# Optimization experiments

Measured on AMD Instinct MI355X. Metric: run time of the kernel, lower is better.

## Reference

```python
import jax, jax.numpy as jnp
import numpy as np
import math

D_MODEL = 128      # embedding_dim
D_STATE = 64
D_CONV = 4
NHEADS = 4         # d_inner / headdim (Mamba2 default headdim=64)
HEADDIM = 64
D_INNER = 256      # expand * d_model
CONV_DIM = 384     # d_inner + 2*ngroups*d_state (ngroups=1)
D_IN_PROJ = 644    # 2*d_inner + 2*ngroups*d_state + nheads
NLAYERS = 2
INPUT_DIM = 768
EPS = 1e-5


def setup_inputs() -> dict:
    key = jax.random.key(0)
    ks = jax.random.split(key, 20)
    rn = lambda k, s, sd=0.02: jax.random.normal(k, s, jnp.float32) * sd
    return {
        "x": jax.random.normal(ks[0], (16, 1024, INPUT_DIM), jnp.float32),
        "fc1_W": rn(ks[1], (INPUT_DIM, D_MODEL)),
        "fc1_b": jnp.zeros((D_MODEL,), jnp.float32),
        "ln_w": jnp.ones((NLAYERS, D_MODEL), jnp.float32),
        "ln_b": jnp.zeros((NLAYERS, D_MODEL), jnp.float32),
        "in_W": rn(ks[2], (NLAYERS, D_MODEL, D_IN_PROJ)),
        "conv_w": rn(ks[3], (NLAYERS, D_CONV, CONV_DIM), 0.1),
        "conv_b": jnp.zeros((NLAYERS, CONV_DIM), jnp.float32),
        "dt_bias": rn(ks[4], (NLAYERS, NHEADS), 0.5),
        "A_log": jnp.log(jax.random.uniform(ks[5], (NLAYERS, NHEADS), jnp.float32, 1.0, 16.0)),
        "Dp": jnp.ones((NLAYERS, NHEADS), jnp.float32),
        "rms_w": jnp.ones((NLAYERS, D_INNER), jnp.float32),
        "out_W": rn(ks[6], (NLAYERS, D_INNER, D_MODEL)),
        "fc2_W1": rn(ks[7], (D_MODEL, D_MODEL)),
        "fc2_b1": jnp.zeros((D_MODEL,), jnp.float32),
        "fc2_W2": rn(ks[8], (D_MODEL, 6)),
        "fc2_b2": jnp.zeros((6,), jnp.float32),
    }


def _pos_embedding(L):
    pos = jnp.arange(L, dtype=jnp.float32)[:, None]                       # (L,1)
    div = jnp.exp(jnp.arange(0, D_MODEL, 2, dtype=jnp.float32) * (-math.log(10000.0) / D_MODEL))
    pe = jnp.zeros((L, D_MODEL), jnp.float32)
    pe = pe.at[:, 0::2].set(jnp.sin(pos * div))
    pe = pe.at[:, 1::2].set(jnp.cos(pos * div))
    return pe[None]                                                        # (1,L,D)


def _layernorm(x, w, b):
    mu = jnp.mean(x, -1, keepdims=True)
    var = jnp.mean(jnp.square(x - mu), -1, keepdims=True)
    return (x - mu) * jax.lax.rsqrt(var + EPS) * w + b


def _mamba2(u, in_W, conv_w, conv_b, dt_bias, A_log, Dp, rms_w, out_W):
    b, l, _ = u.shape
    zxbcdt = u @ in_W                                                      # (b,l,644)
    z = zxbcdt[..., :D_INNER]
    xBC = zxbcdt[..., D_INNER:D_INNER + CONV_DIM]
    dt = jax.nn.softplus(zxbcdt[..., D_INNER + CONV_DIM:] + dt_bias)       # (b,l,h)
    # causal depthwise conv1d (width 4) + SiLU
    xp = jnp.pad(xBC, ((0, 0), (D_CONV - 1, 0), (0, 0)))
    xc = conv_b
    for k in range(D_CONV):
        xc = xc + conv_w[k] * xp[:, k:k + l, :]
    xc = jax.nn.silu(xc)                                                   # (b,l,384)
    xh = xc[..., :D_INNER].reshape(b, l, NHEADS, HEADDIM)                  # (b,l,h,p)
    B = xc[..., D_INNER:D_INNER + D_STATE]                                 # (b,l,n)
    C = xc[..., D_INNER + D_STATE:]                                        # (b,l,n)
    A = -jnp.exp(A_log)                                                    # (h,)
    dA = jnp.exp(dt * A)                                                   # (b,l,h)
    dtx = dt[..., None] * xh                                               # (b,l,h,p)

    def step(h, inp):
        dA_t, dtx_t, B_t, C_t = inp                                        # (b,h),(b,h,p),(b,n),(b,n)
        h = dA_t[..., None, None] * h + dtx_t[..., None] * B_t[:, None, None, :]
        y = jnp.einsum('bhpn,bn->bhp', h, C_t)
        return h, y

    h0 = jnp.zeros((b, NHEADS, HEADDIM, D_STATE), u.dtype)
    _, ys = jax.lax.scan(step, h0, (dA.transpose(1, 0, 2), dtx.transpose(1, 0, 2, 3),
                                    B.transpose(1, 0, 2), C.transpose(1, 0, 2)))
    y = ys.transpose(1, 0, 2, 3) + Dp[None, None, :, None] * xh            # (b,l,h,p)
    y = y.reshape(b, l, D_INNER)
    # gated RMSNorm: rmsnorm(y * silu(z)) * weight
    y = y * jax.nn.silu(z)
    y = y * jax.lax.rsqrt(jnp.mean(jnp.square(y), -1, keepdims=True) + EPS) * rms_w
    return y @ out_W


def reference(x, fc1_W, fc1_b, ln_w, ln_b, in_W, conv_w, conv_b, dt_bias,
              A_log, Dp, rms_w, out_W, fc2_W1, fc2_b1, fc2_W2, fc2_b2):
    h = x @ fc1_W + fc1_b                                                  # (b,l,128)
    h = h + _pos_embedding(h.shape[1])
    for i in range(NLAYERS):
        res = h
        hn = _layernorm(h, ln_w[i], ln_b[i])
        h = _mamba2(hn, in_W[i], conv_w[i], conv_b[i], dt_bias[i],
                    A_log[i], Dp[i], rms_w[i], out_W[i]) + res
        # dropout: identity in eval mode
    h = jax.nn.leaky_relu(h @ fc2_W1 + fc2_b1, negative_slope=0.1)
    return h @ fc2_W2 + fc2_b2                                             # (b,l,6)
```

## Files before the change

### kernel.cpp

```cpp
#include <hip/hip_runtime.h>
#include <hip/hip_bf16.h>

#define BATCH 16
#define SEQ 1024
#define NROWS (BATCH*SEQ)
#define IN_DIM 768
#define DM 128
#define DIP 644
#define DI 256
#define CDIM 384
#define DST 64
#define NH 4
#define HD 64
#define CHUNK 64
#define NCHUNK (SEQ/CHUNK)

#define WB_FC1   0
#define WB_IN    98304
#define WB_OUT   263168
#define WB_FC2   328704
#define WB_TOTAL 345088

typedef __attribute__((ext_vector_type(8))) short short8;
typedef __attribute__((ext_vector_type(4))) float float4v;

__device__ __forceinline__ short f2b(float f) {
    unsigned u = __builtin_bit_cast(unsigned, f);
    u += 0x7fffu + ((u >> 16) & 1u);
    return (short)(u >> 16);
}
__device__ __forceinline__ float s2f(short s) {
    unsigned u = ((unsigned)(unsigned short)s) << 16;
    return __builtin_bit_cast(float, u);
}
__device__ __forceinline__ float silu(float a) { return a / (1.f + expf(-a)); }

__global__ void prep_weights(const float* __restrict__ fc1_W, const float* __restrict__ in_W,
                             const float* __restrict__ out_W, const float* __restrict__ fc2_W1,
                             short* __restrict__ wb) {
    int idx = blockIdx.x * 256 + threadIdx.x;
    if (idx < 98304) {
        int n = idx / 768, k = idx % 768;
        wb[WB_FC1 + idx] = f2b(fc1_W[k * 128 + n]);
        return;
    }
    idx -= 98304;
    if (idx < 2 * 82432) {
        int l = idx / 82432, r = idx % 82432;
        int n = r / 128, k = r % 128;
        wb[WB_IN + idx] = f2b(in_W[(size_t)l * 82432 + k * 644 + n]);
        return;
    }
    idx -= 164864;
    if (idx < 2 * 32768) {
        int l = idx / 32768, r = idx % 32768;
        int n = r / 256, k = r % 256;
        wb[WB_OUT + idx] = f2b(out_W[(size_t)l * 32768 + k * 128 + n]);
        return;
    }
    idx -= 65536;
    if (idx < 16384) {
        int n = idx / 128, k = idx % 128;
        wb[WB_FC2 + idx] = f2b(fc2_W1[k * 128 + n]);
    }
}

#define GEMM_PROLOGUE() \
    int tid = threadIdx.x; \
    int lane = tid & 63; \
    int m = lane & 15; \
    int kq = (lane >> 4) * 8; \
    int w = tid >> 6; \
    int mrow = (w & 3) * 16; \
    int ngrp = w >> 2; \
    int a_off = (mrow + m) * 72 + kq; \
    int b_off = (ngrp * 64 + m) * 72 + kq; \
    int ar = tid >> 3; \
    int ak = (tid & 7) * 8; \
    (void)ar; (void)ak; \
    float4v acc[4]; \
    acc[0] = (float4v)0.f; acc[1] = (float4v)0.f; acc[2] = (float4v)0.f; acc[3] = (float4v)0.f;

#define GEMM_COMPUTE_TILE() \
    { \
        short8 a0 = *reinterpret_cast<const short8*>(&As[a_off]); \
        short8 a1 = *reinterpret_cast<const short8*>(&As[a_off + 32]); \
        _Pragma("unroll") \
        for (int nt = 0; nt < 4; nt++) { \
            short8 b0 = *reinterpret_cast<const short8*>(&Bt[b_off + nt * 16 * 72]); \
            short8 b1 = *reinterpret_cast<const short8*>(&Bt[b_off + nt * 16 * 72 + 32]); \
            acc[nt] = __builtin_amdgcn_mfma_f32_16x16x32_bf16(a0, b0, acc[nt], 0, 0, 0); \
            acc[nt] = __builtin_amdgcn_mfma_f32_16x16x32_bf16(a1, b1, acc[nt], 0, 0, 0); \
        } \
    }

__global__ __launch_bounds__(512) void fc1_mfma(const float* __restrict__ x,
                                                const short* __restrict__ wt,
                                                const float* __restrict__ bias,
                                                const float* __restrict__ lnw0,
                                                const float* __restrict__ lnb0,
                                                float* __restrict__ h,
                                                short* __restrict__ hnb) {
    __shared__ short As[2][32 * 72];
    __shared__ short Bt[2][128 * 72];
    __shared__ float ps1[32][4], ps2[32][4];
    int tid = threadIdx.x;
    int lane = tid & 63;
    int m = lane & 15;
    int quad = lane >> 4;
    int kq = quad * 8;
    int w = tid >> 6;
    int mrow = (w & 1) * 16;
    int ngrp = w >> 1;
    int ar = tid >> 4;
    int ac = (tid & 15) * 4;
    int row0 = blockIdx.x * 32;
    float4v acc[2];
    acc[0] = (float4v)0.f; acc[1] = (float4v)0.f;

#define FC1_STAGE(BI, KT) { \
        const float* src = x + (size_t)(row0 + ar) * IN_DIM + (KT) * 64 + ac; \
        float4 v = *(const float4*)src; \
        short4 pv; pv.x = f2b(v.x); pv.y = f2b(v.y); pv.z = f2b(v.z); pv.w = f2b(v.w); \
        *reinterpret_cast<short4*>(&As[BI][ar * 72 + ac]) = pv; \
        _Pragma("unroll") \
        for (int i = 0; i < 2; i++) { \
            int idx = tid + i * 512; \
            int n = idx >> 3, kk = (idx & 7) * 8; \
            *reinterpret_cast<short8*>(&Bt[BI][n * 72 + kk]) = \
                *reinterpret_cast<const short8*>(&wt[n * 768 + (KT) * 64 + kk]); \
        } }

    FC1_STAGE(0, 0)
    __syncthreads();
    int buf = 0;
    for (int kt = 0; kt < 12; kt++) {
        int nb = buf ^ 1;
        if (kt < 11) FC1_STAGE(nb, kt + 1)
        short8 a0 = *reinterpret_cast<const short8*>(&As[buf][(mrow + m) * 72 + kq]);
        short8 a1 = *reinterpret_cast<const short8*>(&As[buf][(mrow + m) * 72 + kq + 32]);
        #pragma unroll
        for (int nt = 0; nt < 2; nt++) {
            int bo = (ngrp * 32 + nt * 16 + m) * 72 + kq;
            short8 b0 = *reinterpret_cast<const short8*>(&Bt[buf][bo]);
            short8 b1 = *reinterpret_cast<const short8*>(&Bt[buf][bo + 32]);
            acc[nt] = __builtin_amdgcn_mfma_f32_16x16x32_bf16(a0, b0, acc[nt], 0, 0, 0);
            acc[nt] = __builtin_amdgcn_mfma_f32_16x16x32_bf16(a1, b1, acc[nt], 0, 0, 0);
        }
        __syncthreads();
        buf = nb;
    }
    float val[2][4];
    float s1r[4] = {0.f,0.f,0.f,0.f}, s2r[4] = {0.f,0.f,0.f,0.f};
    #pragma unroll
    for (int nt = 0; nt < 2; nt++) {
        int col = ngrp * 32 + nt * 16 + m;
        float bv = bias[col];
        float div = expf(-(float)(col & ~1) * 0.071955784f);
        #pragma unroll
        for (int r = 0; r < 4; r++) {
            int row = row0 + mrow + quad * 4 + r;
            int t = row & (SEQ - 1);
            float arg = (float)t * div;
            float pe = (col & 1) ? cosf(arg) : sinf(arg);
            float v = acc[nt][r] + bv + pe;
            val[nt][r] = v;
            s1r[r] += v; s2r[r] += v * v;
        }
    }
    #pragma unroll
    for (int o = 1; o < 16; o <<= 1) {
        #pragma unroll
        for (int r = 0; r < 4; r++) {
            s1r[r] += __shfl_xor(s1r[r], o);
            s2r[r] += __shfl_xor(s2r[r], o);
        }
    }
    if (m == 0) {
        #pragma unroll
        for (int r = 0; r < 4; r++) {
            ps1[mrow + quad * 4 + r][ngrp] = s1r[r];
            ps2[mrow + quad * 4 + r][ngrp] = s2r[r];
        }
    }
    __syncthreads();
    #pragma unroll
    for (int r = 0; r < 4; r++) {
        int rl = mrow + quad * 4 + r;
        float s1 = ps1[rl][0] + ps1[rl][1] + ps1[rl][2] + ps1[rl][3];
        float s2 = ps2[rl][0] + ps2[rl][1] + ps2[rl][2] + ps2[rl][3];
        float mu = s1 * (1.f / 128.f);
        float rs = rsqrtf(s2 * (1.f / 128.f) - mu * mu + 1e-5f);
        int row = row0 + rl;
        #pragma unroll
        for (int nt = 0; nt < 2; nt++) {
            int col = ngrp * 32 + nt * 16 + m;
            float v = val[nt][r];
            h[(size_t)row * DM + col] = v;
            hnb[(size_t)row * DM + col] = f2b((v - mu) * rs * lnw0[col] + lnb0[col]);
        }
    }
}

__global__ __launch_bounds__(512) void inproj_mfma(const short* __restrict__ hnb,
                                                   const short* __restrict__ wb,
                                                   short* __restrict__ zb,
                                                   short* __restrict__ xbc,
                                                   int layer) {
    __shared__ short As[64 * 72];
    __shared__ short Bt[128 * 72];
    GEMM_PROLOGUE();
    int row0 = blockIdx.x * 64;
    int ncol0 = blockIdx.y * 128;
    const short* wt = wb + WB_IN + (size_t)layer * 82432;
    for (int kt = 0; kt < 2; kt++) {
        int k0 = kt * 64;
        if (kt) __syncthreads();
        *reinterpret_cast<short8*>(&As[ar * 72 + ak]) =
            *reinterpret_cast<const short8*>(&hnb[(size_t)(row0 + ar) * DM + k0 + ak]);
        #pragma unroll
        for (int i = 0; i < 2; i++) {
            int idx = tid + i * 512;
            int n = idx >> 3, kk = (idx & 7) * 8;
            *reinterpret_cast<short8*>(&Bt[n * 72 + kk]) =
                *reinterpret_cast<const short8*>(&wt[(ncol0 + n) * 128 + k0 + kk]);
        }
        __syncthreads();
        GEMM_COMPUTE_TILE();
    }
    int colbase = ncol0 + ngrp * 64;
    if (ncol0 < DI) {
        #pragma unroll
        for (int nt = 0; nt < 4; nt++) {
            int col = colbase + nt * 16 + m;
            #pragma unroll
            for (int r = 0; r < 4; r++) {
                int row = row0 + mrow + (lane >> 4) * 4 + r;
                zb[(size_t)row * DI + col] = f2b(acc[nt][r]);
            }
        }
    } else {
        int xbase = colbase - DI;
        #pragma unroll
        for (int nt = 0; nt < 4; nt++) {
            int col = xbase + nt * 16 + m;
            #pragma unroll
            for (int r = 0; r < 4; r++) {
                int row = row0 + mrow + (lane >> 4) * 4 + r;
                xbc[(size_t)row * CDIM + col] = f2b(acc[nt][r]);
            }
        }
    }
}

__global__ void conv_kernel(const short* __restrict__ xbc,
                            const float* __restrict__ convw, const float* __restrict__ convb,
                            short* __restrict__ xcb,
                            const short* __restrict__ hnb, const short* __restrict__ wb,
                            const float* __restrict__ dt_bias, float* __restrict__ dtb,
                            int layer) {
    int c = threadIdx.x;
    int row0 = blockIdx.x * 4;
    int l0 = row0 & (SEQ - 1);
    const float* cw = convw + (size_t)layer * 4 * CDIM;
    float w0 = cw[c], w1 = cw[CDIM + c], w2 = cw[2 * CDIM + c], w3 = cw[3 * CDIM + c];
    float bb = convb[layer * CDIM + c];
    float v[7];
    #pragma unroll
    for (int i = 0; i < 7; i++) {
        int rr = row0 + i - 3;
        v[i] = (l0 + i - 3 >= 0) ? s2f(xbc[(size_t)rr * CDIM + c]) : 0.f;
    }
    #pragma unroll
    for (int j = 0; j < 4; j++) {
        float acc = bb + w0 * v[j] + w1 * v[j + 1] + w2 * v[j + 2] + w3 * v[j + 3];
        xcb[(size_t)(row0 + j) * CDIM + c] = f2b(silu(acc));
    }
    if (c < 128) {
        int r = c >> 5;
        int rem = c & 31;
        int hh = rem >> 3;
        int part = rem & 7;
        const short* hrow = hnb + (size_t)(row0 + r) * DM + part * 16;
        const short* wrow = wb + WB_IN + (size_t)layer * 82432 + (640 + hh) * 128 + part * 16;
        short8 hv0 = *reinterpret_cast<const short8*>(hrow);
        short8 hv1 = *reinterpret_cast<const short8*>(hrow + 8);
        short8 wv0 = *reinterpret_cast<const short8*>(wrow);
        short8 wv1 = *reinterpret_cast<const short8*>(wrow + 8);
        float s = 0.f;
        #pragma unroll
        for (int q = 0; q < 8; q++)
            s += s2f(hv0[q]) * s2f(wv0[q]) + s2f(hv1[q]) * s2f(wv1[q]);
        s += __shfl_xor(s, 1);
        s += __shfl_xor(s, 2);
        s += __shfl_xor(s, 4);
        if (part == 0) {
            float raw = s + dt_bias[layer * NH + hh];
            float dt = (raw > 20.f) ? raw : log1pf(expf(raw));
            dtb[(size_t)(row0 + r) * NH + hh] = dt;
        }
    }
}

__global__ __launch_bounds__(256) void chunk_state_mfma(const short* __restrict__ xcb,
                                                        const float* __restrict__ dtb,
                                                        const float* __restrict__ A_log,
                                                        short* __restrict__ Slocb,
                                                        float* __restrict__ decay, int layer) {
    __shared__ short XTw[64 * 72];
    __shared__ short BT[64 * 72];
    __shared__ float wst[64];
    int bid = blockIdx.x;
    int c  = bid & (NCHUNK - 1);
    int hh = (bid >> 4) & (NH - 1);
    int b  = bid >> 6;
    int tid = threadIdx.x;
    int row0 = b * SEQ + c * CHUNK;
    float A = -expf(A_log[layer * NH + hh]);

    if (tid < CHUNK) {
        float dtv = dtb[(size_t)(row0 + tid) * NH + hh];
        float l = dtv * A;
        #pragma unroll
        for (int o = 1; o < 64; o <<= 1) { float v = __shfl_up(l, o); if (tid >= o) l += v; }
        float Ltot = __shfl(l, 63);
        wst[tid] = expf(Ltot - l) * dtv;
        if (tid == 63) decay[bid] = expf(Ltot);
    }
    __syncthreads();
    {
        int p = tid & 63;
        int tb0 = tid >> 6;
        #pragma unroll
        for (int i = 0; i < 2; i++) {
            int t0 = (tb0 + i * 4) * 8;
            short8 xv, bv;
            #pragma unroll
            for (int j = 0; j < 8; j++) {
                int t = t0 + j;
                const short* xr = xcb + (size_t)(row0 + t) * CDIM;
                xv[j] = f2b(s2f(xr[hh * HD + p]) * wst[t]);
                bv[j] = xr[DI + p];
            }
            *reinterpret_cast<short8*>(&XTw[p * 72 + t0]) = xv;
            *reinterpret_cast<short8*>(&BT[p * 72 + t0]) = bv;
        }
    }
    __syncthreads();

    int lane = tid & 63;
    int m = lane & 15;
    int kq = (lane >> 4) * 8;
    int w = tid >> 6;
    int a_off = (w * 16 + m) * 72 + kq;
    float4v acc[4];
    acc[0] = (float4v)0.f; acc[1] = (float4v)0.f; acc[2] = (float4v)0.f; acc[3] = (float4v)0.f;
    short8 a0 = *reinterpret_cast<const short8*>(&XTw[a_off]);
    short8 a1 = *reinterpret_cast<const short8*>(&XTw[a_off + 32]);
    #pragma unroll
    for (int nt = 0; nt < 4; nt++) {
        int bo = (nt * 16 + m) * 72 + kq;
        short8 b0 = *reinterpret_cast<const short8*>(&BT[bo]);
        short8 b1 = *reinterpret_cast<const short8*>(&BT[bo + 32]);
        acc[nt] = __builtin_amdgcn_mfma_f32_16x16x32_bf16(a0, b0, acc[nt], 0, 0, 0);
        acc[nt] = __builtin_amdgcn_mfma_f32_16x16x32_bf16(a1, b1, acc[nt], 0, 0, 0);
    }
    short* Sp = Slocb + (size_t)bid * (HD * DST);
    int tq = (lane >> 4) * 4;
    #pragma unroll
    for (int nt = 0; nt < 4; nt++) {
        #pragma unroll
        for (int r = 0; r < 4; r++) {
            int p = w * 16 + tq + r;
            int n = nt * 16 + m;
            Sp[p * DST + n] = f2b(acc[nt][r]);
        }
    }
}

__global__ __launch_bounds__(256) void chunk_out_mfma(const short* __restrict__ xcb,
                                                      const float* __restrict__ dtb,
                                                      const float* __restrict__ A_log,
                                                      const float* __restrict__ Dpw,
                                                      const short* __restrict__ Slocb,
                                                      const float* __restrict__ decay,
                                                      short* __restrict__ ybb, int layer) {
    __shared__ short Cb[64 * 72];
    __shared__ short Bb[64 * 72];
    __shared__ short XT[64 * 72];
    __shared__ short HT[64 * 72];
    __shared__ float Ls[64], dts[64];
    int bid = blockIdx.x;
    int c  = bid & (NCHUNK - 1);
    int hh = (bid >> 4) & (NH - 1);
    int b  = bid >> 6;
    int tid = threadIdx.x;
    int row0 = b * SEQ + c * CHUNK;
    int bh0 = bid & ~(NCHUNK - 1);
    float A = -expf(A_log[layer * NH + hh]);
    float Dph = Dpw[layer * NH + hh];

    if (tid < CHUNK) {
        float dtv = dtb[(size_t)(row0 + tid) * NH + hh];
        float l = dtv * A;
        #pragma unroll
        for (int o = 1; o < 64; o <<= 1) { float v = __shfl_up(l, o); if (tid >= o) l += v; }
        Ls[tid] = l;
        dts[tid] = dtv;
    }
    {
        float hreg[16];
        #pragma unroll
        for (int k = 0; k < 16; k++) hreg[k] = 0.f;
        for (int j = 0; j < c; j++) {
            float d = decay[bh0 + j];
            const short* Sp = Slocb + (size_t)(bh0 + j) * (HD * DST) + tid * 16;
            short8 s0 = *reinterpret_cast<const short8*>(Sp);
            short8 s1 = *reinterpret_cast<const short8*>(Sp + 8);
            #pragma unroll
            for (int k = 0; k < 8; k++) {
                hreg[k]     = d * hreg[k]     + s2f(s0[k]);
                hreg[8 + k] = d * hreg[8 + k] + s2f(s1[k]);
            }
        }
        int p = tid >> 2;
        int n0 = (tid & 3) * 16;
        short8 h0, h1;
        #pragma unroll
        for (int k = 0; k < 8; k++) { h0[k] = f2b(hreg[k]); h1[k] = f2b(hreg[8 + k]); }
        *reinterpret_cast<short8*>(&HT[p * 72 + n0]) = h0;
        *reinterpret_cast<short8*>(&HT[p * 72 + n0 + 8]) = h1;
    }
    {
        int p = tid & 63;
        int tb0 = tid >> 6;
        #pragma unroll
        for (int i = 0; i < 2; i++) {
            int t0 = (tb0 + i * 4) * 8;
            short8 xv;
            #pragma unroll
            for (int j = 0; j < 8; j++)
                xv[j] = xcb[(size_t)(row0 + t0 + j) * CDIM + hh * HD + p];
            *reinterpret_cast<short8*>(&XT[p * 72 + t0]) = xv;
        }
    }
    #pragma unroll
    for (int i = 0; i < 2; i++) {
        int idx = tid + i * 256;
        int t = idx >> 3, cb = (idx & 7) * 8;
        const short* xr = xcb + (size_t)(row0 + t) * CDIM;
        *reinterpret_cast<short8*>(&Bb[t * 72 + cb]) =
            *reinterpret_cast<const short8*>(&xr[DI + cb]);
        *reinterpret_cast<short8*>(&Cb[t * 72 + cb]) =
            *reinterpret_cast<const short8*>(&xr[DI + DST + cb]);
    }
    __syncthreads();

    int lane = tid & 63;
    int m = lane & 15;
    int kq = (lane >> 4) * 8;
    int w = tid >> 6;
    int tq = (lane >> 4) * 4;
    int a_off = (w * 16 + m) * 72 + kq;

    short8 ca0 = *reinterpret_cast<const short8*>(&Cb[a_off]);
    short8 ca1 = *reinterpret_cast<const short8*>(&Cb[a_off + 32]);

    float4v g[4], ir[4];
    #pragma unroll
    for (int i = 0; i < 4; i++) { g[i] = (float4v)0.f; ir[i] = (float4v)0.f; }
    #pragma unroll
    for (int st = 0; st < 4; st++) {
        int bo = (st * 16 + m) * 72 + kq;
        short8 b0 = *reinterpret_cast<const short8*>(&Bb[bo]);
        short8 b1 = *reinterpret_cast<const short8*>(&Bb[bo + 32]);
        g[st] = __builtin_amdgcn_mfma_f32_16x16x32_bf16(ca0, b0, g[st], 0, 0, 0);
        g[st] = __builtin_amdgcn_mfma_f32_16x16x32_bf16(ca1, b1, g[st], 0, 0, 0);
        short8 h0 = *reinterpret_cast<const short8*>(&HT[bo]);
        short8 h1 = *reinterpret_cast<const short8*>(&HT[bo + 32]);
        ir[st] = __builtin_amdgcn_mfma_f32_16x16x32_bf16(ca0, h0, ir[st], 0, 0, 0);
        ir[st] = __builtin_amdgcn_mfma_f32_16x16x32_bf16(ca1, h1, ir[st], 0, 0, 0);
    }
    __syncthreads();
    #pragma unroll
    for (int st = 0; st < 4; st++) {
        #pragma unroll
        for (int r = 0; r < 4; r++) {
            int t = w * 16 + tq + r;
            int s = st * 16 + m;
            float mv = 0.f;
            if (s <= t) mv = g[st][r] * expf(Ls[t] - Ls[s]) * dts[s];
            Bb[t * 72 + s] = f2b(mv);
        }
    }
    __syncthreads();
    float4v yi[4];
    #pragma unroll
    for (int i = 0; i < 4; i++) yi[i] = (float4v)0.f;
    short8 ma0 = *reinterpret_cast<const short8*>(&Bb[a_off]);
    short8 ma1 = *reinterpret_cast<const short8*>(&Bb[a_off + 32]);
    #pragma unroll
    for (int pt = 0; pt < 4; pt++) {
        int bo = (pt * 16 + m) * 72 + kq;
        short8 x0 = *reinterpret_cast<const short8*>(&XT[bo]);
        short8 x1 = *reinterpret_cast<const short8*>(&XT[bo + 32]);
        yi[pt] = __builtin_amdgcn_mfma_f32_16x16x32_bf16(ma0, x0, yi[pt], 0, 0, 0);
        yi[pt] = __builtin_amdgcn_mfma_f32_16x16x32_bf16(ma1, x1, yi[pt], 0, 0, 0);
    }
    #pragma unroll
    for (int r = 0; r < 4; r++) {
        int t = w * 16 + tq + r;
        float et = expf(Ls[t]);
        short* yr = ybb + (size_t)(row0 + t) * DI + hh * HD;
        #pragma unroll
        for (int pt = 0; pt < 4; pt++) {
            int p = pt * 16 + m;
            float xv = s2f(XT[p * 72 + t]);
            yr[p] = f2b(yi[pt][r] + et * ir[pt][r] + Dph * xv);
        }
    }
}

__global__ __launch_bounds__(512) void outproj_gate_mfma(const short* __restrict__ ybb,
                                                         const short* __restrict__ zb,
                                                         const float* __restrict__ rmsw,
                                                         const short* __restrict__ wb,
                                                         const float* __restrict__ lnw2,
                                                         const float* __restrict__ lnb2,
                                                         float* __restrict__ h,
                                                         short* __restrict__ hnb,
                                                         const float* __restrict__ fc2_b1,
                                                         const float* __restrict__ fc2_W2,
                                                         const float* __restrict__ fc2_b2,
                                                         float* __restrict__ outp,
                                                         int layer, int do_fc2) {
    __shared__ __align__(16) short As[32 * 264];
    __shared__ __align__(16) short Bt[2][128 * 72];
    __shared__ float w2s[768];
    int tid = threadIdx.x;
    int lane = tid & 63;
    int m = lane & 15;
    int quad = lane >> 4;
    int kq = quad * 8;
    int w = tid >> 6;
    int mrow = (w & 1) * 16;
    int ngrp = w >> 1;
    int row0 = blockIdx.x * 32;
    const short* wt = wb + WB_OUT + (size_t)layer * 32768;
    if (do_fc2)
        for (int i = tid; i < 768; i += 512) w2s[i] = fc2_W2[i];
    {
        int r = tid >> 4, j = tid & 15;
        const short* yr = ybb + (size_t)(row0 + r) * DI + j * 16;
        const short* zr = zb + (size_t)(row0 + r) * DI + j * 16;
        short8 y0 = *reinterpret_cast<const short8*>(yr);
        short8 y1 = *reinterpret_cast<const short8*>(yr + 8);
        short8 z0 = *reinterpret_cast<const short8*>(zr);
        short8 z1 = *reinterpret_cast<const short8*>(zr + 8);
        float v[16]; float s2 = 0.f;
        #pragma unroll
        for (int q = 0; q < 8; q++) {
            v[q]     = s2f(y0[q]) * silu(s2f(z0[q]));
            v[8 + q] = s2f(y1[q]) * silu(s2f(z1[q]));
        }
        #pragma unroll
        for (int q = 0; q < 16; q++) s2 += v[q] * v[q];
        #pragma unroll
        for (int o = 1; o < 16; o <<= 1) s2 += __shfl_xor(s2, o);
        float rs = rsqrtf(s2 * (1.f / 256.f) + 1e-5f);
        const float* rw = rmsw + layer * DI + j * 16;
        short8 a0, a1;
        #pragma unroll
        for (int q = 0; q < 8; q++) {
            a0[q] = f2b(v[q] * rs * rw[q]);
            a1[q] = f2b(v[8 + q] * rs * rw[8 + q]);
        }
        *reinterpret_cast<short8*>(&As[r * 264 + j * 16]) = a0;
        *reinterpret_cast<short8*>(&As[r * 264 + j * 16 + 8]) = a1;
    }
    {
        int n = tid >> 2, kk = (tid & 3) * 16;
        *reinterpret_cast<short8*>(&Bt[0][n * 72 + kk]) =
            *reinterpret_cast<const short8*>(&wt[n * 256 + kk]);
        *reinterpret_cast<short8*>(&Bt[0][n * 72 + kk + 8]) =
            *reinterpret_cast<const short8*>(&wt[n * 256 + kk + 8]);
    }
    __syncthreads();
    float4v acc[2];
    acc[0] = (float4v)0.f; acc[1] = (float4v)0.f;
    int buf = 0;
    for (int kt = 0; kt < 4; kt++) {
        if (kt < 3) {
            int n = tid >> 2, kk = (tid & 3) * 16;
            *reinterpret_cast<short8*>(&Bt[buf ^ 1][n * 72 + kk]) =
                *reinterpret_cast<const short8*>(&wt[n * 256 + (kt + 1) * 64 + kk]);
            *reinterpret_cast<short8*>(&Bt[buf ^ 1][n * 72 + kk + 8]) =
                *reinterpret_cast<const short8*>(&wt[n * 256 + (kt + 1) * 64 + kk + 8]);
        }
        short8 a0 = *reinterpret_cast<const short8*>(&As[(mrow + m) * 264 + kt * 64 + kq]);
        short8 a1 = *reinterpret_cast<const short8*>(&As[(mrow + m) * 264 + kt * 64 + kq + 32]);
        #pragma unroll
        for (int nt = 0; nt < 2; nt++) {
            int bo = (ngrp * 32 + nt * 16 + m) * 72 + kq;
            short8 b0 = *reinterpret_cast<const short8*>(&Bt[buf][bo]);
            short8 b1 = *reinterpret_cast<const short8*>(&Bt[buf][bo + 32]);
            acc[nt] = __builtin_amdgcn_mfma_f32_16x16x32_bf16(a0, b0, acc[nt], 0, 0, 0);
            acc[nt] = __builtin_amdgcn_mfma_f32_16x16x32_bf16(a1, b1, acc[nt], 0, 0, 0);
        }
        __syncthreads();
        buf ^= 1;
    }
    float* hs = (float*)As;
    #pragma unroll
    for (int nt = 0; nt < 2; nt++) {
        int col = ngrp * 32 + nt * 16 + m;
        #pragma unroll
        for (int r = 0; r < 4; r++)
            hs[(mrow + quad * 4 + r) * 132 + col] = acc[nt][r];
    }
    __syncthreads();
    int er = tid >> 4, ej = tid & 15;
    int erow = row0 + er;
    float vals[8];
    float s1 = 0.f, s2v = 0.f;
    {
        const float* hsrc = h + (size_t)erow * DM + ej * 8;
        float4 h0 = *(const float4*)hsrc;
        float4 h1 = *(const float4*)(hsrc + 4);
        const float* hrow = &hs[er * 132 + ej * 8];
        float4 q0 = *(const float4*)hrow;
        float4 q1 = *(const float4*)(hrow + 4);
        vals[0] = h0.x + q0.x; vals[1] = h0.y + q0.y; vals[2] = h0.z + q0.z; vals[3] = h0.w + q0.w;
        vals[4] = h1.x + q1.x; vals[5] = h1.y + q1.y; vals[6] = h1.z + q1.z; vals[7] = h1.w + q1.w;
        #pragma unroll
        for (int i = 0; i < 8; i++) { s1 += vals[i]; s2v += vals[i] * vals[i]; }
    }
    if (!do_fc2) {
        #pragma unroll
        for (int o = 1; o < 16; o <<= 1) { s1 += __shfl_xor(s1, o); s2v += __shfl_xor(s2v, o); }
        float* hdst = h + (size_t)erow * DM + ej * 8;
        *(float4*)hdst = make_float4(vals[0], vals[1], vals[2], vals[3]);
        *(float4*)(hdst + 4) = make_float4(vals[4], vals[5], vals[6], vals[7]);
        float mu = s1 * (1.f / 128.f);
        float rs2 = rsqrtf(s2v * (1.f / 128.f) - mu * mu + 1e-5f);
        const float* lw = lnw2 + ej * 8;
        const float* lb = lnb2 + ej * 8;
        short8 a0;
        #pragma unroll
        for (int i = 0; i < 8; i++) a0[i] = f2b((vals[i] - mu) * rs2 * lw[i] + lb[i]);
        *reinterpret_cast<short8*>(hnb + (size_t)erow * DM + ej * 8) = a0;
        return;
    }
    __syncthreads();
    short* As2 = (short*)As;
    {
        short8 ap;
        #pragma unroll
        for (int i = 0; i < 8; i++) ap[i] = f2b(vals[i]);
        *reinterpret_cast<short8*>(&As2[er * 136 + ej * 8]) = ap;
    }
    const short* wtf = wb + WB_FC2;
    short* Bt2 = (short*)Bt;
    {
        int n = tid >> 2, kk = (tid & 3) * 32;
        #pragma unroll
        for (int i = 0; i < 4; i++)
            *reinterpret_cast<short8*>(&Bt2[n * 136 + kk + i * 8]) =
                *reinterpret_cast<const short8*>(&wtf[n * 128 + kk + i * 8]);
    }
    __syncthreads();
    float4v acc2[2];
    acc2[0] = (float4v)0.f; acc2[1] = (float4v)0.f;
    #pragma unroll
    for (int kt = 0; kt < 2; kt++) {
        int k0 = kt * 64;
        short8 a0 = *reinterpret_cast<const short8*>(&As2[(mrow + m) * 136 + k0 + kq]);
        short8 a1 = *reinterpret_cast<const short8*>(&As2[(mrow + m) * 136 + k0 + kq + 32]);
        #pragma unroll
        for (int nt = 0; nt < 2; nt++) {
            int bo = (ngrp * 32 + nt * 16 + m) * 136 + k0 + kq;
            short8 b0 = *reinterpret_cast<const short8*>(&Bt2[bo]);
            short8 b1 = *reinterpret_cast<const short8*>(&Bt2[bo + 32]);
            acc2[nt] = __builtin_amdgcn_mfma_f32_16x16x32_bf16(a0, b0, acc2[nt], 0, 0, 0);
            acc2[nt] = __builtin_amdgcn_mfma_f32_16x16x32_bf16(a1, b1, acc2[nt], 0, 0, 0);
        }
    }
    __syncthreads();
    float* h2s = (float*)As;
    #pragma unroll
    for (int nt = 0; nt < 2; nt++) {
        int col = ngrp * 32 + nt * 16 + m;
        float bv = fc2_b1[col];
        #pragma unroll
        for (int r = 0; r < 4; r++) {
            float o = acc2[nt][r] + bv;
            h2s[(mrow + quad * 4 + r) * 132 + col] = (o > 0.f) ? o : 0.1f * o;
        }
    }
    __syncthreads();
    if (tid < 384) {
        int r = tid / 12, q = tid % 12, cc = q >> 1, part = q & 1;
        float a2 = 0.f;
        #pragma unroll 8
        for (int k = 0; k < 64; k++)
            a2 += h2s[r * 132 + part * 64 + k] * w2s[(part * 64 + k) * 6 + cc];
        a2 += __shfl_xor(a2, 1);
        if (!part) outp[(size_t)(row0 + r) * 6 + cc] = fc2_b2[cc] + a2;
    }
}

extern "C" void kernel_launch(void* const* d_in, const int* in_sizes, int n_in,
                              void* d_out, int out_size, void* d_ws, size_t ws_size,
                              hipStream_t stream) {
    const float* x       = (const float*)d_in[0];
    const float* fc1_W   = (const float*)d_in[1];
    const float* fc1_b   = (const float*)d_in[2];
    const float* ln_w    = (const float*)d_in[3];
    const float* ln_b    = (const float*)d_in[4];
    const float* in_W    = (const float*)d_in[5];
    const float* conv_w  = (const float*)d_in[6];
    const float* conv_b  = (const float*)d_in[7];
    const float* dt_bias = (const float*)d_in[8];
    const float* A_log   = (const float*)d_in[9];
    const float* Dp      = (const float*)d_in[10];
    const float* rms_w   = (const float*)d_in[11];
    const float* out_W   = (const float*)d_in[12];
    const float* fc2_W1  = (const float*)d_in[13];
    const float* fc2_b1  = (const float*)d_in[14];
    const float* fc2_W2  = (const float*)d_in[15];
    const float* fc2_b2  = (const float*)d_in[16];
    float* out = (float*)d_out;

    float* ws = (float*)d_ws;
    float* h     = ws;
    float* dtb   = h     + (size_t)NROWS * DM;
    float* decay = dtb   + (size_t)NROWS * NH;
    short* sbase = (short*)(decay + 1024);
    short* hnb   = sbase;
    short* zb    = hnb   + (size_t)NROWS * DM;
    short* xbc   = zb    + (size_t)NROWS * DI;
    short* xcb   = xbc   + (size_t)NROWS * CDIM;
    short* ybb   = xcb   + (size_t)NROWS * CDIM;
    short* Slocb = ybb   + (size_t)NROWS * DI;
    short* wb    = Slocb + (size_t)BATCH*NH*NCHUNK*HD*DST;

    prep_weights<<<1348, 256, 0, stream>>>(fc1_W, in_W, out_W, fc2_W1, wb);
    fc1_mfma<<<NROWS / 32, 512, 0, stream>>>(x, wb + WB_FC1, fc1_b, ln_w, ln_b, h, hnb);

    for (int layer = 0; layer < 2; layer++) {
        inproj_mfma<<<dim3(NROWS / 64, 5), 512, 0, stream>>>(hnb, wb, zb, xbc, layer);
        conv_kernel<<<NROWS / 4, CDIM, 0, stream>>>(xbc, conv_w, conv_b, xcb,
                                                    hnb, wb, dt_bias, dtb, layer);
        chunk_state_mfma<<<BATCH*NH*NCHUNK, 256, 0, stream>>>(xcb, dtb, A_log, Slocb, decay, layer);
        chunk_out_mfma<<<BATCH*NH*NCHUNK, 256, 0, stream>>>(xcb, dtb, A_log, Dp, Slocb, decay,
                                                            ybb, layer);
        outproj_gate_mfma<<<NROWS / 32, 512, 0, stream>>>(ybb, zb, rms_w, wb,
                                                          ln_w + DM, ln_b + DM, h, hnb,
                                                          fc2_b1, fc2_W2, fc2_b2, out,
                                                          layer, layer == 1 ? 1 : 0);
    }
}
```

Before: 247.1 us.

## Fuse depthwise conv into chunk kernels and dt projection into in-proj GEMM

```diff
diff --git a/kernel.cpp b/kernel.cpp
--- a/kernel.cpp
+++ b/kernel.cpp
@@ -206,6 +206,8 @@
                                                    const short* __restrict__ wb,
                                                    short* __restrict__ zb,
                                                    short* __restrict__ xbc,
+                                                   float* __restrict__ dtb,
+                                                   const float* __restrict__ dt_bias,
                                                    int layer) {
     __shared__ short As[64 * 72];
     __shared__ short Bt[128 * 72];
@@ -251,60 +253,34 @@
             }
         }
     }
-}
-
-__global__ void conv_kernel(const short* __restrict__ xbc,
-                            const float* __restrict__ convw, const float* __restrict__ convb,
-                            short* __restrict__ xcb,
-                            const short* __restrict__ hnb, const short* __restrict__ wb,
-                            const float* __restrict__ dt_bias, float* __restrict__ dtb,
-                            int layer) {
-    int c = threadIdx.x;
-    int row0 = blockIdx.x * 4;
-    int l0 = row0 & (SEQ - 1);
-    const float* cw = convw + (size_t)layer * 4 * CDIM;
-    float w0 = cw[c], w1 = cw[CDIM + c], w2 = cw[2 * CDIM + c], w3 = cw[3 * CDIM + c];
-    float bb = convb[layer * CDIM + c];
-    float v[7];
-    #pragma unroll
-    for (int i = 0; i < 7; i++) {
-        int rr = row0 + i - 3;
-        v[i] = (l0 + i - 3 >= 0) ? s2f(xbc[(size_t)rr * CDIM + c]) : 0.f;
-    }
-    #pragma unroll
-    for (int j = 0; j < 4; j++) {
-        float acc = bb + w0 * v[j] + w1 * v[j + 1] + w2 * v[j + 2] + w3 * v[j + 3];
-        xcb[(size_t)(row0 + j) * CDIM + c] = f2b(silu(acc));
-    }
-    if (c < 128) {
-        int r = c >> 5;
-        int rem = c & 31;
-        int hh = rem >> 3;
-        int part = rem & 7;
-        const short* hrow = hnb + (size_t)(row0 + r) * DM + part * 16;
-        const short* wrow = wb + WB_IN + (size_t)layer * 82432 + (640 + hh) * 128 + part * 16;
-        short8 hv0 = *reinterpret_cast<const short8*>(hrow);
-        short8 hv1 = *reinterpret_cast<const short8*>(hrow + 8);
-        short8 wv0 = *reinterpret_cast<const short8*>(wrow);
-        short8 wv1 = *reinterpret_cast<const short8*>(wrow + 8);
+    if (ncol0 == 0) {
+        int r = tid >> 3;
+        int rem = tid & 7;
+        int hh2 = rem >> 1, half = rem & 1;
+        const short* hrow = hnb + (size_t)(row0 + r) * DM + half * 64;
+        const short* wrow = wt + (640 + hh2) * 128 + half * 64;
         float s = 0.f;
         #pragma unroll
-        for (int q = 0; q < 8; q++)
-            s += s2f(hv0[q]) * s2f(wv0[q]) + s2f(hv1[q]) * s2f(wv1[q]);
+        for (int i = 0; i < 8; i++) {
+            short8 hv = *reinterpret_cast<const short8*>(hrow + i * 8);
+            short8 wv = *reinterpret_cast<const short8*>(wrow + i * 8);
+            #pragma unroll
+            for (int q = 0; q < 8; q++) s += s2f(hv[q]) * s2f(wv[q]);
+        }
         s += __shfl_xor(s, 1);
-        s += __shfl_xor(s, 2);
-        s += __shfl_xor(s, 4);
-        if (part == 0) {
-            float raw = s + dt_bias[layer * NH + hh];
+        if (half == 0) {
+            float raw = s + dt_bias[layer * NH + hh2];
             float dt = (raw > 20.f) ? raw : log1pf(expf(raw));
-            dtb[(size_t)(row0 + r) * NH + hh] = dt;
-        }
-    }
-}
-
-__global__ __launch_bounds__(256) void chunk_state_mfma(const short* __restrict__ xcb,
+            dtb[(size_t)(row0 + r) * NH + hh2] = dt;
+        }
+    }
+}
+
+__global__ __launch_bounds__(256) void chunk_state_mfma(const short* __restrict__ xbc,
                                                         const float* __restrict__ dtb,
                                                         const float* __restrict__ A_log,
+                                                        const float* __restrict__ convw,
+                                                        const float* __restrict__ convb,
                                                         short* __restrict__ Slocb,
                                                         float* __restrict__ decay, int layer) {
     __shared__ short XTw[64 * 72];
@@ -330,21 +306,40 @@
     __syncthreads();
     {
         int p = tid & 63;
-        int tb0 = tid >> 6;
-        #pragma unroll
-        for (int i = 0; i < 2; i++) {
-            int t0 = (tb0 + i * 4) * 8;
-            short8 xv, bv;
-            #pragma unroll
-            for (int j = 0; j < 8; j++) {
-                int t = t0 + j;
-                const short* xr = xcb + (size_t)(row0 + t) * CDIM;
-                xv[j] = f2b(s2f(xr[hh * HD + p]) * wst[t]);
-                bv[j] = xr[DI + p];
-            }
-            *reinterpret_cast<short8*>(&XTw[p * 72 + t0]) = xv;
-            *reinterpret_cast<short8*>(&BT[p * 72 + t0]) = bv;
-        }
+        int grp = tid >> 6;
+        int t0 = grp * 16;
+        int cx = hh * HD + p;
+        int cb2 = DI + p;
+        const float* cw = convw + (size_t)layer * 4 * CDIM;
+        float wx0 = cw[cx], wx1 = cw[CDIM + cx], wx2 = cw[2 * CDIM + cx], wx3 = cw[3 * CDIM + cx];
+        float bxc = convb[layer * CDIM + cx];
+        float wb0 = cw[cb2], wb1 = cw[CDIM + cb2], wb2 = cw[2 * CDIM + cb2], wb3 = cw[3 * CDIM + cb2];
+        float bbc = convb[layer * CDIM + cb2];
+        bool ok = (c | t0) != 0;
+        const short* xb = xbc + (size_t)row0 * CDIM;
+        float vx0 = ok ? s2f(xb[(t0 - 3) * CDIM + cx]) : 0.f;
+        float vx1 = ok ? s2f(xb[(t0 - 2) * CDIM + cx]) : 0.f;
+        float vx2 = ok ? s2f(xb[(t0 - 1) * CDIM + cx]) : 0.f;
+        float vb0 = ok ? s2f(xb[(t0 - 3) * CDIM + cb2]) : 0.f;
+        float vb1 = ok ? s2f(xb[(t0 - 2) * CDIM + cb2]) : 0.f;
+        float vb2 = ok ? s2f(xb[(t0 - 1) * CDIM + cb2]) : 0.f;
+        short8 xv0, xv1, bv0, bv1;
+        #pragma unroll
+        for (int j = 0; j < 16; j++) {
+            float vx3 = s2f(xb[(t0 + j) * CDIM + cx]);
+            float vb3 = s2f(xb[(t0 + j) * CDIM + cb2]);
+            float ax = bxc + wx0 * vx0 + wx1 * vx1 + wx2 * vx2 + wx3 * vx3;
+            float ab = bbc + wb0 * vb0 + wb1 * vb1 + wb2 * vb2 + wb3 * vb3;
+            short sx = f2b(silu(ax) * wst[t0 + j]);
+            short sb = f2b(silu(ab));
+            if (j < 8) { xv0[j] = sx; bv0[j] = sb; } else { xv1[j - 8] = sx; bv1[j - 8] = sb; }
+            vx0 = vx1; vx1 = vx2; vx2 = vx3;
+            vb0 = vb1; vb1 = vb2; vb2 = vb3;
+        }
+        *reinterpret_cast<short8*>(&XTw[p * 72 + t0]) = xv0;
+        *reinterpret_cast<short8*>(&XTw[p * 72 + t0 + 8]) = xv1;
+        *reinterpret_cast<short8*>(&BT[p * 72 + t0]) = bv0;
+        *reinterpret_cast<short8*>(&BT[p * 72 + t0 + 8]) = bv1;
     }
     __syncthreads();
 
@@ -378,10 +373,12 @@
     }
 }
 
-__global__ __launch_bounds__(256) void chunk_out_mfma(const short* __restrict__ xcb,
+__global__ __launch_bounds__(256) void chunk_out_mfma(const short* __restrict__ xbc,
                                                       const float* __restrict__ dtb,
                                                       const float* __restrict__ A_log,
                                                       const float* __restrict__ Dpw,
+                                                      const float* __restrict__ convw,
+                                                      const float* __restrict__ convb,
                                                       const short* __restrict__ Slocb,
                                                       const float* __restrict__ decay,
                                                       short* __restrict__ ybb, int layer) {
@@ -433,26 +430,50 @@
     }
     {
         int p = tid & 63;
-        int tb0 = tid >> 6;
-        #pragma unroll
-        for (int i = 0; i < 2; i++) {
-            int t0 = (tb0 + i * 4) * 8;
-            short8 xv;
-            #pragma unroll
-            for (int j = 0; j < 8; j++)
-                xv[j] = xcb[(size_t)(row0 + t0 + j) * CDIM + hh * HD + p];
-            *reinterpret_cast<short8*>(&XT[p * 72 + t0]) = xv;
-        }
-    }
-    #pragma unroll
-    for (int i = 0; i < 2; i++) {
-        int idx = tid + i * 256;
-        int t = idx >> 3, cb = (idx & 7) * 8;
-        const short* xr = xcb + (size_t)(row0 + t) * CDIM;
-        *reinterpret_cast<short8*>(&Bb[t * 72 + cb]) =
-            *reinterpret_cast<const short8*>(&xr[DI + cb]);
-        *reinterpret_cast<short8*>(&Cb[t * 72 + cb]) =
-            *reinterpret_cast<const short8*>(&xr[DI + DST + cb]);
+        int grp = tid >> 6;
+        int t0 = grp * 16;
+        int cx = hh * HD + p;
+        const float* cw = convw + (size_t)layer * 4 * CDIM;
+        float w0 = cw[cx], w1 = cw[CDIM + cx], w2 = cw[2 * CDIM + cx], w3 = cw[3 * CDIM + cx];
+        float bc = convb[layer * CDIM + cx];
+        bool ok = (c | t0) != 0;
+        const short* xb = xbc + (size_t)row0 * CDIM;
+        float v0 = ok ? s2f(xb[(t0 - 3) * CDIM + cx]) : 0.f;
+        float v1 = ok ? s2f(xb[(t0 - 2) * CDIM + cx]) : 0.f;
+        float v2 = ok ? s2f(xb[(t0 - 1) * CDIM + cx]) : 0.f;
+        short8 o0, o1;
+        #pragma unroll
+        for (int j = 0; j < 16; j++) {
+            float v3 = s2f(xb[(t0 + j) * CDIM + cx]);
+            float a = bc + w0 * v0 + w1 * v1 + w2 * v2 + w3 * v3;
+            short sv = f2b(silu(a));
+            if (j < 8) o0[j] = sv; else o1[j - 8] = sv;
+            v0 = v1; v1 = v2; v2 = v3;
+        }
+        *reinterpret_cast<short8*>(&XT[p * 72 + t0]) = o0;
+        *reinterpret_cast<short8*>(&XT[p * 72 + t0 + 8]) = o1;
+    }
+    {
+        int n = tid & 127;
+        int tg = tid >> 7;
+        int t0 = tg * 32;
+        int colg = DI + n;
+        const float* cw = convw + (size_t)layer * 4 * CDIM;
+        float w0 = cw[colg], w1 = cw[CDIM + colg], w2 = cw[2 * CDIM + colg], w3 = cw[3 * CDIM + colg];
+        float bc = convb[layer * CDIM + colg];
+        bool ok = (c | t0) != 0;
+        const short* xb = xbc + (size_t)row0 * CDIM;
+        float v0 = ok ? s2f(xb[(t0 - 3) * CDIM + colg]) : 0.f;
+        float v1 = ok ? s2f(xb[(t0 - 2) * CDIM + colg]) : 0.f;
+        float v2 = ok ? s2f(xb[(t0 - 1) * CDIM + colg]) : 0.f;
+        short* dst = (n < 64) ? &Bb[n] : &Cb[n - 64];
+        #pragma unroll 8
+        for (int j = 0; j < 32; j++) {
+            float v3 = s2f(xb[(t0 + j) * CDIM + colg]);
+            float a = bc + w0 * v0 + w1 * v1 + w2 * v2 + w3 * v3;
+            dst[(t0 + j) * 72] = f2b(silu(a));
+            v0 = v1; v1 = v2; v2 = v3;
+        }
     }
     __syncthreads();
 
@@ -739,8 +760,7 @@
     short* hnb   = sbase;
     short* zb    = hnb   + (size_t)NROWS * DM;
     short* xbc   = zb    + (size_t)NROWS * DI;
-    short* xcb   = xbc   + (size_t)NROWS * CDIM;
-    short* ybb   = xcb   + (size_t)NROWS * CDIM;
+    short* ybb   = xbc   + (size_t)NROWS * CDIM;
     short* Slocb = ybb   + (size_t)NROWS * DI;
     short* wb    = Slocb + (size_t)BATCH*NH*NCHUNK*HD*DST;
 
@@ -748,12 +768,12 @@
     fc1_mfma<<<NROWS / 32, 512, 0, stream>>>(x, wb + WB_FC1, fc1_b, ln_w, ln_b, h, hnb);
 
     for (int layer = 0; layer < 2; layer++) {
-        inproj_mfma<<<dim3(NROWS / 64, 5), 512, 0, stream>>>(hnb, wb, zb, xbc, layer);
-        conv_kernel<<<NROWS / 4, CDIM, 0, stream>>>(xbc, conv_w, conv_b, xcb,
-                                                    hnb, wb, dt_bias, dtb, layer);
-        chunk_state_mfma<<<BATCH*NH*NCHUNK, 256, 0, stream>>>(xcb, dtb, A_log, Slocb, decay, layer);
-        chunk_out_mfma<<<BATCH*NH*NCHUNK, 256, 0, stream>>>(xcb, dtb, A_log, Dp, Slocb, decay,
-                                                            ybb, layer);
+        inproj_mfma<<<dim3(NROWS / 64, 5), 512, 0, stream>>>(hnb, wb, zb, xbc,
+                                                             dtb, dt_bias, layer);
+        chunk_state_mfma<<<BATCH*NH*NCHUNK, 256, 0, stream>>>(xbc, dtb, A_log, conv_w, conv_b,
+                                                              Slocb, decay, layer);
+        chunk_out_mfma<<<BATCH*NH*NCHUNK, 256, 0, stream>>>(xbc, dtb, A_log, Dp, conv_w, conv_b,
+                                                            Slocb, decay, ybb, layer);
         outproj_gate_mfma<<<NROWS / 32, 512, 0, stream>>>(ybb, zb, rms_w, wb,
                                                           ln_w + DM, ln_b + DM, h, hnb,
                                                           fc2_b1, fc2_W2, fc2_b2, out,
```

After: 262.9 us. 1.06x slower.

## Fuse causal conv1d and dt projection into the in-projection GEMM epilogue

Applied to the files above, without the earlier changes.

```diff
diff --git a/kernel.cpp b/kernel.cpp
--- a/kernel.cpp
+++ b/kernel.cpp
@@ -205,10 +205,16 @@
 __global__ __launch_bounds__(512) void inproj_mfma(const short* __restrict__ hnb,
                                                    const short* __restrict__ wb,
                                                    short* __restrict__ zb,
-                                                   short* __restrict__ xbc,
+                                                   short* __restrict__ xcb,
+                                                   float* __restrict__ dtb,
+                                                   const float* __restrict__ dt_bias,
+                                                   const float* __restrict__ convw,
+                                                   const float* __restrict__ convb,
                                                    int layer) {
-    __shared__ short As[64 * 72];
-    __shared__ short Bt[128 * 72];
+    __shared__ __align__(16) char smem[27648];
+    short* As = (short*)smem;
+    short* Bt = (short*)(smem + 9216);
+    short* Xt = (short*)smem;
     GEMM_PROLOGUE();
     int row0 = blockIdx.x * 64;
     int ncol0 = blockIdx.y * 128;
@@ -228,8 +234,8 @@
         __syncthreads();
         GEMM_COMPUTE_TILE();
     }
-    int colbase = ncol0 + ngrp * 64;
     if (ncol0 < DI) {
+        int colbase = ncol0 + ngrp * 64;
         #pragma unroll
         for (int nt = 0; nt < 4; nt++) {
             int col = colbase + nt * 16 + m;
@@ -239,65 +245,84 @@
                 zb[(size_t)row * DI + col] = f2b(acc[nt][r]);
             }
         }
+        if (ncol0 == 0) {
+            int r = tid >> 3;
+            int rem = tid & 7;
+            int hh2 = rem >> 1, half = rem & 1;
+            const short* hrow = hnb + (size_t)(row0 + r) * DM + half * 64;
+            const short* wrow = wt + (640 + hh2) * 128 + half * 64;
+            float s = 0.f;
+            #pragma unroll
+            for (int i = 0; i < 8; i++) {
+                short8 hv = *reinterpret_cast<const short8*>(hrow + i * 8);
+                short8 wv = *reinterpret_cast<const short8*>(wrow + i * 8);
+                #pragma unroll
+                for (int q = 0; q < 8; q++) s += s2f(hv[q]) * s2f(wv[q]);
+            }
+            s += __shfl_xor(s, 1);
+            if (half == 0) {
+                float raw = s + dt_bias[layer * NH + hh2];
+                float dt = (raw > 20.f) ? raw : log1pf(expf(raw));
+                dtb[(size_t)(row0 + r) * NH + hh2] = dt;
+            }
+        }
     } else {
-        int xbase = colbase - DI;
+        int xcol0 = ncol0 - DI;
+        __syncthreads();
         #pragma unroll
         for (int nt = 0; nt < 4; nt++) {
-            int col = xbase + nt * 16 + m;
+            int col = ngrp * 64 + nt * 16 + m;
             #pragma unroll
             for (int r = 0; r < 4; r++) {
-                int row = row0 + mrow + (lane >> 4) * 4 + r;
-                xbc[(size_t)row * CDIM + col] = f2b(acc[nt][r]);
+                int tr = mrow + (lane >> 4) * 4 + r;
+                Xt[(3 + tr) * 136 + col] = f2b(acc[nt][r]);
             }
         }
-    }
-}
-
-__global__ void conv_kernel(const short* __restrict__ xbc,
-                            const float* __restrict__ convw, const float* __restrict__ convb,
-                            short* __restrict__ xcb,
-                            const short* __restrict__ hnb, const short* __restrict__ wb,
-                            const float* __restrict__ dt_bias, float* __restrict__ dtb,
-                            int layer) {
-    int c = threadIdx.x;
-    int row0 = blockIdx.x * 4;
-    int l0 = row0 & (SEQ - 1);
-    const float* cw = convw + (size_t)layer * 4 * CDIM;
-    float w0 = cw[c], w1 = cw[CDIM + c], w2 = cw[2 * CDIM + c], w3 = cw[3 * CDIM + c];
-    float bb = convb[layer * CDIM + c];
-    float v[7];
-    #pragma unroll
-    for (int i = 0; i < 7; i++) {
-        int rr = row0 + i - 3;
-        v[i] = (l0 + i - 3 >= 0) ? s2f(xbc[(size_t)rr * CDIM + c]) : 0.f;
-    }
-    #pragma unroll
-    for (int j = 0; j < 4; j++) {
-        float acc = bb + w0 * v[j] + w1 * v[j + 1] + w2 * v[j + 2] + w3 * v[j + 3];
-        xcb[(size_t)(row0 + j) * CDIM + c] = f2b(silu(acc));
-    }
-    if (c < 128) {
-        int r = c >> 5;
-        int rem = c & 31;
-        int hh = rem >> 3;
-        int part = rem & 7;
-        const short* hrow = hnb + (size_t)(row0 + r) * DM + part * 16;
-        const short* wrow = wb + WB_IN + (size_t)layer * 82432 + (640 + hh) * 128 + part * 16;
-        short8 hv0 = *reinterpret_cast<const short8*>(hrow);
-        short8 hv1 = *reinterpret_cast<const short8*>(hrow + 8);
-        short8 wv0 = *reinterpret_cast<const short8*>(wrow);
-        short8 wv1 = *reinterpret_cast<const short8*>(wrow + 8);
-        float s = 0.f;
-        #pragma unroll
-        for (int q = 0; q < 8; q++)
-            s += s2f(hv0[q]) * s2f(wv0[q]) + s2f(hv1[q]) * s2f(wv1[q]);
-        s += __shfl_xor(s, 1);
-        s += __shfl_xor(s, 2);
-        s += __shfl_xor(s, 4);
-        if (part == 0) {
-            float raw = s + dt_bias[layer * NH + hh];
-            float dt = (raw > 20.f) ? raw : log1pf(expf(raw));
-            dtb[(size_t)(row0 + r) * NH + hh] = dt;
+        bool seqstart = (row0 & (SEQ - 1)) == 0;
+        if (tid < 384) {
+            int hr = tid >> 7;
+            int col = tid & 127;
+            short hv = 0;
+            if (!seqstart) {
+                const short* hrow = hnb + (size_t)(row0 - 3 + hr) * DM;
+                const short* wrow = wt + (ncol0 + col) * 128;
+                float s = 0.f;
+                #pragma unroll
+                for (int i = 0; i < 16; i++) {
+                    short8 h8 = *reinterpret_cast<const short8*>(hrow + i * 8);
+                    short8 w8 = *reinterpret_cast<const short8*>(wrow + i * 8);
+                    #pragma unroll
+                    for (int q = 0; q < 8; q++) s += s2f(h8[q]) * s2f(w8[q]);
+                }
+                hv = f2b(s);
+            }
+            Xt[hr * 136 + col] = hv;
+        }
+        __syncthreads();
+        int c8 = (tid & 15) * 8;
+        const float* cw = convw + (size_t)layer * 4 * CDIM + xcol0 + c8;
+        const float* cbp = convb + layer * CDIM + xcol0 + c8;
+        float w0[8], w1[8], w2[8], w3[8], bb[8];
+        #pragma unroll
+        for (int q = 0; q < 8; q++) {
+            w0[q] = cw[q]; w1[q] = cw[CDIM + q]; w2[q] = cw[2 * CDIM + q]; w3[q] = cw[3 * CDIM + q];
+            bb[q] = cbp[q];
+        }
+        #pragma unroll
+        for (int pass = 0; pass < 2; pass++) {
+            int t = pass * 32 + (tid >> 4);
+            short8 r0 = *reinterpret_cast<const short8*>(&Xt[(t + 0) * 136 + c8]);
+            short8 r1 = *reinterpret_cast<const short8*>(&Xt[(t + 1) * 136 + c8]);
+            short8 r2 = *reinterpret_cast<const short8*>(&Xt[(t + 2) * 136 + c8]);
+            short8 r3 = *reinterpret_cast<const short8*>(&Xt[(t + 3) * 136 + c8]);
+            short8 out;
+            #pragma unroll
+            for (int q = 0; q < 8; q++) {
+                float a = bb[q] + w0[q] * s2f(r0[q]) + w1[q] * s2f(r1[q])
+                        + w2[q] * s2f(r2[q]) + w3[q] * s2f(r3[q]);
+                out[q] = f2b(silu(a));
+            }
+            *reinterpret_cast<short8*>(&xcb[(size_t)(row0 + t) * CDIM + xcol0 + c8]) = out;
         }
     }
 }
@@ -738,8 +763,7 @@
     short* sbase = (short*)(decay + 1024);
     short* hnb   = sbase;
     short* zb    = hnb   + (size_t)NROWS * DM;
-    short* xbc   = zb    + (size_t)NROWS * DI;
-    short* xcb   = xbc   + (size_t)NROWS * CDIM;
+    short* xcb   = zb    + (size_t)NROWS * DI;
     short* ybb   = xcb   + (size_t)NROWS * CDIM;
     short* Slocb = ybb   + (size_t)NROWS * DI;
     short* wb    = Slocb + (size_t)BATCH*NH*NCHUNK*HD*DST;
@@ -748,9 +772,9 @@
     fc1_mfma<<<NROWS / 32, 512, 0, stream>>>(x, wb + WB_FC1, fc1_b, ln_w, ln_b, h, hnb);
 
     for (int layer = 0; layer < 2; layer++) {
-        inproj_mfma<<<dim3(NROWS / 64, 5), 512, 0, stream>>>(hnb, wb, zb, xbc, layer);
-        conv_kernel<<<NROWS / 4, CDIM, 0, stream>>>(xbc, conv_w, conv_b, xcb,
-                                                    hnb, wb, dt_bias, dtb, layer);
+        inproj_mfma<<<dim3(NROWS / 64, 5), 512, 0, stream>>>(hnb, wb, zb, xcb,
+                                                             dtb, dt_bias,
+                                                             conv_w, conv_b, layer);
         chunk_state_mfma<<<BATCH*NH*NCHUNK, 256, 0, stream>>>(xcb, dtb, A_log, Slocb, decay, layer);
         chunk_out_mfma<<<BATCH*NH*NCHUNK, 256, 0, stream>>>(xcb, dtb, A_log, Dp, Slocb, decay,
                                                             ybb, layer);
```

New measurement: 262.2 us. 1.06x slower.
